# Performance work log

Measured on AMD Instinct MI355X. Metric: run time of the kernel, lower is better.

Reference implementation:

```python
import jax, jax.numpy as jnp
import numpy as np

B, C, Z, E = 2, 32, 4, 2
N = C * C * Z  # 4096 grid points per element
P_TH, T_TH = 0.5, 0.5
ELE_D = (0.74, 0.528)


def _consts():
    real_size = jnp.array([25.0, 25.0, 3.0], jnp.float32)
    lattice = real_size / jnp.array([C, C, Z], jnp.float32)
    g = jnp.stack(jnp.meshgrid(jnp.arange(C), jnp.arange(C), jnp.arange(Z), indexing='ij'), axis=-1)
    pit = g.reshape(N, 3).astype(jnp.float32)
    return pit, lattice


def _cdist(a, b):
    # a [M,3], b [K,3] -> [M,K] euclidean distance
    d2 = jnp.sum((a[:, None, :] - b[None, :, :]) ** 2, axis=-1)
    return jnp.sqrt(d2)


def _nms(pos, conf, valid, ele_d):
    # Fixed-shape version of Analyzer.nms: sort by confidence desc (invalid -> -inf, sorts last),
    # triu(<d) adjacency restricted to valid points, matrix-multiply suppression correction.
    key = jnp.where(valid, conf, -jnp.inf)
    order = jnp.argsort(-key)              # descending confidence
    pos_s = pos[order]
    valid_s = valid[order]
    dist = _cdist(pos_s, pos_s)            # [N,N] ~ 64 MB
    iu = jnp.triu(jnp.ones((N, N), bool), k=1)
    adj = ((dist < ele_d) & iu & valid_s[:, None] & valid_s[None, :]).astype(pos.dtype)
    restrain = adj.sum(0)                  # col sums: # earlier neighbors
    restrain_one = (restrain != 0).astype(pos.dtype)
    correct = restrain_one @ adj           # earlier neighbors that are themselves suppressed
    sel = ((restrain - correct) == 0) & valid_s
    keep = jnp.zeros(N, bool).at[order].set(sel)
    return keep & valid


def _match(t_pos, t_valid, p_pos, p_valid, ele_d):
    # TP matching: T point is matched if any valid P within ele_d; argmin gives its P partner.
    dist = _cdist(t_pos, p_pos)            # [N,N]
    dist = jnp.where(t_valid[:, None] & p_valid[None, :], dist, jnp.inf)
    tp_t_mask = (dist < ele_d).any(1)      # rows in torch's TP_T_index
    tp_p_idx = jnp.argmin(dist, axis=1).astype(jnp.int32)  # torch's TP_P_index (valid where tp_t_mask)
    return tp_t_mask, tp_p_idx


def setup_inputs() -> dict:
    key = jax.random.key(0)
    k1, k2 = jax.random.split(key)
    predictions = jax.random.uniform(k1, (B, C, C, Z, E, 4), jnp.float32)
    targets = jax.random.uniform(k2, (B, C, C, Z, E, 4), jnp.float32)
    return {"predictions": predictions, "targets": targets}


def reference(predictions, targets):
    pit, lattice = _consts()
    # [B,C,C,Z,E,4] -> [B,E,N,4]
    pred = predictions.reshape(B, C, C, Z, E, 4).transpose(0, 4, 1, 2, 3, 5).reshape(B, E, N, 4)
    tgt = targets.reshape(B, C, C, Z, E, 4).transpose(0, 4, 1, 2, 3, 5).reshape(B, E, N, 4)

    p_pos = (pred[..., :3] + pit) * lattice    # [B,E,N,3] absolute coords
    p_conf = pred[..., 3]
    mask_p = p_conf > P_TH
    t_pos = (tgt[..., :3] + pit) * lattice
    mask_t = tgt[..., 3] > T_TH

    keeps, tpt, tpp, tptn, tppn = [], [], [], [], []
    for e in range(E):
        d = ELE_D[e]
        keep_e = jax.vmap(lambda p, c, v: _nms(p, c, v, d))(p_pos[:, e], p_conf[:, e], mask_p[:, e])
        tt, tp = jax.vmap(lambda tq, tv, pq, pv: _match(tq, tv, pq, pv, d))(
            t_pos[:, e], mask_t[:, e], p_pos[:, e], mask_p[:, e])
        ttn, tpn = jax.vmap(lambda tq, tv, pq, pv: _match(tq, tv, pq, pv, d))(
            t_pos[:, e], mask_t[:, e], p_pos[:, e], keep_e)
        keeps.append(keep_e); tpt.append(tt); tpp.append(tp); tptn.append(ttn); tppn.append(tpn)

    keep_nms = jnp.stack(keeps, 1)   # [B,E,N] combined mask_p & nms keep
    tp_t_mask = jnp.stack(tpt, 1)
    tp_p_idx = jnp.stack(tpp, 1)
    tp_t_mask_nms = jnp.stack(tptn, 1)
    tp_p_idx_nms = jnp.stack(tppn, 1)

    return (p_pos, mask_p, keep_nms, t_pos, mask_t,
            tp_t_mask, tp_p_idx, tp_t_mask_nms, tp_p_idx_nms)
```

## Files before the change

kernel.cpp:

```cpp
#include <hip/hip_runtime.h>
#include <cmath>
#include <cstdint>

namespace {
constexpr int NPT  = 4096;
constexpr int NTOT = 16384;

constexpr int O_PPOS  = 0;
constexpr int O_MASKP = 49152;
constexpr int O_KEEP  = 65536;
constexpr int O_TPOS  = 81920;
constexpr int O_MASKT = 131072;
constexpr int O_TPT   = 147456;
constexpr int O_TPP   = 163840;
constexpr int O_TPTN  = 180224;
constexpr int O_TPPN  = 196608;

constexpr size_t W_RESTR = 0;
constexpr size_t W_KEEP  = 16384;
constexpr size_t W_CNT   = 32768;
constexpr size_t W_LIST  = 33024;

constexpr float GUARD = 1.4999f;
}

__device__ __forceinline__ unsigned long long shfl_xor_u64(unsigned long long v, int m) {
    unsigned lo = (unsigned)v, hi = (unsigned)(v >> 32);
    lo = __shfl_xor(lo, m); hi = __shfl_xor(hi, m);
    return ((unsigned long long)hi << 32) | lo;
}
__device__ __forceinline__ unsigned long long shfl_down_u64(unsigned long long v, int m) {
    unsigned lo = (unsigned)v, hi = (unsigned)(v >> 32);
    lo = __shfl_down(lo, m); hi = __shfl_down(hi, m);
    return ((unsigned long long)hi << 32) | lo;
}

__device__ __forceinline__ float3 cellpos(float4 p, int n) {
#pragma clang fp contract(off)
    float fx = (float)(n >> 7), fy = (float)((n >> 2) & 31), fz = (float)(n & 3);
    float3 r;
    r.x = (p.x + fx) * 0.78125f;
    r.y = (p.y + fy) * 0.78125f;
    r.z = (p.z + fz) * 0.75f;
    return r;
}
__device__ __forceinline__ float dist2(float3 a, float3 b) {
#pragma clang fp contract(off)
    float dx = a.x - b.x, dy = a.y - b.y, dz = a.z - b.z;
    float d2 = dx * dx + dy * dy;
    return d2 + dz * dz;
}

__global__ void __launch_bounds__(256) k_restrain(const float4* __restrict__ pred,
                                                  float* __restrict__ out,
                                                  unsigned char* __restrict__ restru,
                                                  unsigned* __restrict__ cnt,
                                                  float s0, float s1) {
#pragma clang fp contract(off)
    int tid = blockIdx.x * 256 + threadIdx.x;
    if (tid == 0) *cnt = 0u;
    int row = tid >> 1, h = tid & 1;
    int n = row & (NPT - 1), s = row >> 12, b = s >> 1, e = s & 1;
    int base4 = b * 8192 + e;
    float se = (s & 1) ? s1 : s0;
    float4 p = pred[base4 + n * 2];
    float3 pj = cellpos(p, n);
    bool valid = p.w > 0.5f;
    if (h == 0) {
        out[O_PPOS + row * 3 + 0] = pj.x;
        out[O_PPOS + row * 3 + 1] = pj.y;
        out[O_PPOS + row * 3 + 2] = pj.z;
        out[O_MASKP + row] = valid ? 1.0f : 0.0f;
    }
    unsigned c = 0;
    if (valid) {
        int gx = n >> 7, gy = (n >> 2) & 31;
        for (int qq = 0; qq < 5; ++qq) {
            int q = qq * 2 + h;
            if (q > 8) continue;
            int nx = gx + q / 3 - 1, ny = gy + q % 3 - 1;
            if ((unsigned)nx > 31u || (unsigned)ny > 31u) continue;
            int nb = nx * 128 + ny * 4;
#pragma unroll
            for (int nz = 0; nz < 4; ++nz) {
                int ni = nb + nz;
                float4 pi = pred[base4 + ni * 2];
                float3 qi = cellpos(pi, ni);
                float d2 = dist2(pj, qi);
                bool prec = (pi.w > p.w) || ((pi.w == p.w) && (ni < n));
                if ((pi.w > 0.5f) && (d2 < se) && prec) c++;
            }
        }
    }
    c += __shfl_xor(c, 1);
    if (h == 0) restru[row] = (unsigned char)c;
}

__global__ void __launch_bounds__(256) k_suppress(const float4* __restrict__ pred,
                                                  const unsigned char* __restrict__ restru,
                                                  float* __restrict__ out,
                                                  unsigned char* __restrict__ keepu,
                                                  float s0, float s1) {
#pragma clang fp contract(off)
    int tid = blockIdx.x * 256 + threadIdx.x;
    int row = tid >> 1, h = tid & 1;
    int n = row & (NPT - 1), s = row >> 12, b = s >> 1, e = s & 1;
    int base4 = b * 8192 + e, srow = s * NPT;
    float se = (s & 1) ? s1 : s0;
    float4 p = pred[base4 + n * 2];
    float3 pj = cellpos(p, n);
    bool valid = p.w > 0.5f;
    unsigned any = 0;
    if (valid) {
        int gx = n >> 7, gy = (n >> 2) & 31;
        for (int qq = 0; qq < 5; ++qq) {
            int q = qq * 2 + h;
            if (q > 8) continue;
            int nx = gx + q / 3 - 1, ny = gy + q % 3 - 1;
            if ((unsigned)nx > 31u || (unsigned)ny > 31u) continue;
            int nb = nx * 128 + ny * 4;
#pragma unroll
            for (int nz = 0; nz < 4; ++nz) {
                int ni = nb + nz;
                float4 pi = pred[base4 + ni * 2];
                float3 qi = cellpos(pi, ni);
                float d2 = dist2(pj, qi);
                bool prec = (pi.w > p.w) || ((pi.w == p.w) && (ni < n));
                bool flg = (pi.w > 0.5f) && (restru[srow + ni] == 0);
                if (flg && (d2 < se) && prec) any = 1u;
            }
        }
    }
    any |= __shfl_xor(any, 1);
    if (h == 0) {
        bool keep = valid && !any;
        out[O_KEEP + row] = keep ? 1.0f : 0.0f;
        keepu[row] = keep ? 1 : 0;
    }
}

__global__ void __launch_bounds__(256) k_match1(const float4* __restrict__ pred,
                                                const float4* __restrict__ tgt,
                                                const unsigned char* __restrict__ keepu,
                                                float* __restrict__ out,
                                                unsigned* __restrict__ list,
                                                unsigned* __restrict__ cnt,
                                                float s0, float s1) {
#pragma clang fp contract(off)
    int tid = blockIdx.x * 256 + threadIdx.x;
    int row = tid >> 2, h = tid & 3;
    int n = row & (NPT - 1), s = row >> 12, b = s >> 1, e = s & 1;
    int base4 = b * 8192 + e, srow = s * NPT;
    float se = (s & 1) ? s1 : s0;
    float4 t4 = tgt[base4 + n * 2];
    float3 tj = cellpos(t4, n);
    bool tv = t4.w > 0.5f;
    if (h == 0) {
        out[O_TPOS + row * 3 + 0] = tj.x;
        out[O_TPOS + row * 3 + 1] = tj.y;
        out[O_TPOS + row * 3 + 2] = tj.z;
        out[O_MASKT + row] = tv ? 1.0f : 0.0f;
    }
    if (!tv) {
        if (h == 0) {
            out[O_TPT + row] = 0.0f; out[O_TPTN + row] = 0.0f;
            out[O_TPP + row] = 0.0f; out[O_TPPN + row] = 0.0f;
        }
        return;
    }
    int gx = n >> 7, gy = (n >> 2) & 31;
    unsigned long long bs = ~0ull, bn = ~0ull;
    unsigned as_ = 0, an_ = 0;
    for (int qq = 0; qq < 7; ++qq) {
        int q = qq * 4 + h;
        if (q > 24) continue;
        int nx = gx + q / 5 - 2, ny = gy + q % 5 - 2;
        if ((unsigned)nx > 31u || (unsigned)ny > 31u) continue;
        int nb = nx * 128 + ny * 4;
#pragma unroll
        for (int nz = 0; nz < 4; ++nz) {
            int ni = nb + nz;
            float4 pi = pred[base4 + ni * 2];
            float3 qi = cellpos(pi, ni);
            float d2 = dist2(tj, qi);
            float dist = sqrtf(d2);
            unsigned long long enc =
                ((unsigned long long)__float_as_uint(dist) << 32) | (unsigned)ni;
            if (pi.w > 0.5f) { if (enc < bs) bs = enc; if (d2 < se) as_ = 1u; }
            if (keepu[srow + ni]) { if (enc < bn) bn = enc; if (d2 < se) an_ = 1u; }
        }
    }
    for (int m = 1; m < 4; m <<= 1) {
        unsigned long long o = shfl_xor_u64(bs, m); if (o < bs) bs = o;
        o = shfl_xor_u64(bn, m); if (o < bn) bn = o;
        as_ |= __shfl_xor(as_, m);
        an_ |= __shfl_xor(an_, m);
    }
    if (h == 0) {
        out[O_TPT + row]  = as_ ? 1.0f : 0.0f;
        out[O_TPTN + row] = an_ ? 1.0f : 0.0f;
        bool acc_s = __uint_as_float((unsigned)(bs >> 32)) < GUARD;
        bool acc_n = __uint_as_float((unsigned)(bn >> 32)) < GUARD;
        if (acc_s) out[O_TPP + row]  = (float)(unsigned)(bs & 0xffffffffull);
        if (acc_n) out[O_TPPN + row] = (float)(unsigned)(bn & 0xffffffffull);
        if (!acc_s || !acc_n) list[atomicAdd(cnt, 1u)] = (unsigned)row;
    }
}

__global__ void __launch_bounds__(256) k_match2(const float4* __restrict__ pred,
                                                const float4* __restrict__ tgt,
                                                const unsigned char* __restrict__ keepu,
                                                const unsigned* __restrict__ list,
                                                const unsigned* __restrict__ cnt,
                                                float* __restrict__ out) {
#pragma clang fp contract(off)
    __shared__ unsigned long long rs[4], rn[4];
    unsigned C = *cnt;
    for (unsigned r = blockIdx.x; r < C; r += gridDim.x) {
        int row = (int)list[r];
        int n = row & (NPT - 1), s = row >> 12, b = s >> 1, e = s & 1;
        int base4 = b * 8192 + e, srow = s * NPT;
        float4 t4 = tgt[base4 + n * 2];
        float3 tj = cellpos(t4, n);
        unsigned long long bs = ~0ull, bn = ~0ull;
        for (int k = (int)threadIdx.x; k < NPT; k += 256) {
            float4 pi = pred[base4 + k * 2];
            float3 qi = cellpos(pi, k);
            float d2 = dist2(tj, qi);
            float dist = sqrtf(d2);
            unsigned long long enc =
                ((unsigned long long)__float_as_uint(dist) << 32) | (unsigned)k;
            if (pi.w > 0.5f && enc < bs) bs = enc;
            if (keepu[srow + k] && enc < bn) bn = enc;
        }
        for (int m = 32; m; m >>= 1) {
            unsigned long long o = shfl_down_u64(bs, m); if (o < bs) bs = o;
            o = shfl_down_u64(bn, m); if (o < bn) bn = o;
        }
        int w = (int)(threadIdx.x >> 6);
        if ((threadIdx.x & 63) == 0) { rs[w] = bs; rn[w] = bn; }
        __syncthreads();
        if (threadIdx.x == 0) {
            for (int i = 1; i < 4; ++i) {
                if (rs[i] < bs) bs = rs[i];
                if (rn[i] < bn) bn = rn[i];
            }
            unsigned is_ = (bs == ~0ull) ? 0u : (unsigned)(bs & 0xffffffffull);
            unsigned in_ = (bn == ~0ull) ? 0u : (unsigned)(bn & 0xffffffffull);
            out[O_TPP + row]  = (float)is_;
            out[O_TPPN + row] = (float)in_;
        }
        __syncthreads();
    }
}

static float sq_boundary(float t) {
    float f = (float)((double)t * (double)t);
    while (sqrtf(f) >= t) f = nextafterf(f, 0.0f);
    while (sqrtf(f) < t)  f = nextafterf(f, __builtin_inff());
    return f;
}

extern "C" void kernel_launch(void* const* d_in, const int* in_sizes, int n_in,
                              void* d_out, int out_size, void* d_ws, size_t ws_size,
                              hipStream_t stream) {
    (void)in_sizes; (void)n_in; (void)out_size; (void)ws_size;
    const float4* pred = (const float4*)d_in[0];
    const float4* tgt  = (const float4*)d_in[1];
    float* out = (float*)d_out;
    char* ws = (char*)d_ws;

    unsigned char* restru = (unsigned char*)(ws + W_RESTR);
    unsigned char* keepu  = (unsigned char*)(ws + W_KEEP);
    unsigned* cnt  = (unsigned*)(ws + W_CNT);
    unsigned* list = (unsigned*)(ws + W_LIST);

    float s0 = sq_boundary(0.74f);
    float s1 = sq_boundary(0.528f);

    k_restrain<<<dim3(128), dim3(256), 0, stream>>>(pred, out, restru, cnt, s0, s1);
    k_suppress<<<dim3(128), dim3(256), 0, stream>>>(pred, restru, out, keepu, s0, s1);
    k_match1 <<<dim3(256), dim3(256), 0, stream>>>(pred, tgt, keepu, out, list, cnt, s0, s1);
    k_match2 <<<dim3(128), dim3(256), 0, stream>>>(pred, tgt, keepu, list, cnt, out);
}
```

Before: 77.90 us.

## Fuse restrain and suppress into one tiled NMS kernel; inline match fallback

Merges the restrain-count and suppression kernels into one kernel per tile. Each block recomputes restrain counts for its tile plus a one-cell halo in shared memory, so the global restrain buffer and one launch go away. The two match kernels are also merged: rows whose local-neighbourhood best match is not guaranteed now do the full-grid scan in the same 4-lane group instead of being queued with an atomic and handled by a second kernel. This cuts four launches to two, at the cost of redundant halo work and a possibly long serial scan for the rare fallback rows.

```diff
diff --git a/kernel.cpp b/kernel.cpp
--- a/kernel.cpp
+++ b/kernel.cpp
@@ -4,7 +4,6 @@
 
 namespace {
 constexpr int NPT  = 4096;
-constexpr int NTOT = 16384;
 
 constexpr int O_PPOS  = 0;
 constexpr int O_MASKP = 49152;
@@ -16,22 +15,12 @@
 constexpr int O_TPTN  = 180224;
 constexpr int O_TPPN  = 196608;
 
-constexpr size_t W_RESTR = 0;
-constexpr size_t W_KEEP  = 16384;
-constexpr size_t W_CNT   = 32768;
-constexpr size_t W_LIST  = 33024;
-
 constexpr float GUARD = 1.4999f;
 }
 
 __device__ __forceinline__ unsigned long long shfl_xor_u64(unsigned long long v, int m) {
     unsigned lo = (unsigned)v, hi = (unsigned)(v >> 32);
     lo = __shfl_xor(lo, m); hi = __shfl_xor(hi, m);
-    return ((unsigned long long)hi << 32) | lo;
-}
-__device__ __forceinline__ unsigned long long shfl_down_u64(unsigned long long v, int m) {
-    unsigned lo = (unsigned)v, hi = (unsigned)(v >> 32);
-    lo = __shfl_down(lo, m); hi = __shfl_down(hi, m);
     return ((unsigned long long)hi << 32) | lo;
 }
 
@@ -51,36 +40,66 @@
     return d2 + dz * dz;
 }
 
-__global__ void __launch_bounds__(256) k_restrain(const float4* __restrict__ pred,
-                                                  float* __restrict__ out,
-                                                  unsigned char* __restrict__ restru,
-                                                  unsigned* __restrict__ cnt,
-                                                  float s0, float s1) {
-#pragma clang fp contract(off)
-    int tid = blockIdx.x * 256 + threadIdx.x;
-    if (tid == 0) *cnt = 0u;
-    int row = tid >> 1, h = tid & 1;
-    int n = row & (NPT - 1), s = row >> 12, b = s >> 1, e = s & 1;
+__global__ void __launch_bounds__(256) k_nms(const float4* __restrict__ pred,
+                                             float* __restrict__ out,
+                                             unsigned char* __restrict__ keepu,
+                                             float s0, float s1) {
+#pragma clang fp contract(off)
+    __shared__ unsigned char restr[216];
+    int bid = blockIdx.x;
+    int h2 = bid & 1, gx = (bid >> 1) & 31, s = bid >> 6;
+    int b = s >> 1, e = s & 1;
     int base4 = b * 8192 + e;
     float se = (s & 1) ? s1 : s0;
+    int gy0 = h2 << 4;
+    int t = (int)threadIdx.x;
+
+    if (t < 216) {
+        int rgx = t / 72, rem = t - rgx * 72, rgy = rem >> 2, z = rem & 3;
+        int px = gx + rgx - 1, py = gy0 + rgy - 1;
+        unsigned c = 0;
+        if ((unsigned)px < 32u && (unsigned)py < 32u) {
+            int pn = px * 128 + py * 4 + z;
+            float4 p = pred[base4 + pn * 2];
+            if (p.w > 0.5f) {
+                float3 pj = cellpos(p, pn);
+                for (int q = 0; q < 9; ++q) {
+                    int nx = px + q / 3 - 1, ny = py + q % 3 - 1;
+                    if ((unsigned)nx > 31u || (unsigned)ny > 31u) continue;
+                    int nb = nx * 128 + ny * 4;
+#pragma unroll
+                    for (int nz = 0; nz < 4; ++nz) {
+                        int ni = nb + nz;
+                        float4 pi = pred[base4 + ni * 2];
+                        float3 qi = cellpos(pi, ni);
+                        float d2 = dist2(pj, qi);
+                        bool prec = (pi.w > p.w) || ((pi.w == p.w) && (ni < pn));
+                        if ((pi.w > 0.5f) && (d2 < se) && prec) c++;
+                    }
+                }
+            }
+        }
+        restr[t] = (unsigned char)c;
+    }
+    __syncthreads();
+
+    int r = t >> 2, h = t & 3;
+    int gy = gy0 + (r >> 2), z = r & 3;
+    int n = (gx << 7) + (gy << 2) + z;
+    int row = s * NPT + n;
     float4 p = pred[base4 + n * 2];
     float3 pj = cellpos(p, n);
     bool valid = p.w > 0.5f;
-    if (h == 0) {
-        out[O_PPOS + row * 3 + 0] = pj.x;
-        out[O_PPOS + row * 3 + 1] = pj.y;
-        out[O_PPOS + row * 3 + 2] = pj.z;
-        out[O_MASKP + row] = valid ? 1.0f : 0.0f;
-    }
-    unsigned c = 0;
+    unsigned any = 0;
     if (valid) {
-        int gx = n >> 7, gy = (n >> 2) & 31;
-        for (int qq = 0; qq < 5; ++qq) {
-            int q = qq * 2 + h;
+        for (int qq = 0; qq < 3; ++qq) {
+            int q = qq * 4 + h;
             if (q > 8) continue;
-            int nx = gx + q / 3 - 1, ny = gy + q % 3 - 1;
+            int dx = q / 3 - 1, dy = q % 3 - 1;
+            int nx = gx + dx, ny = gy + dy;
             if ((unsigned)nx > 31u || (unsigned)ny > 31u) continue;
             int nb = nx * 128 + ny * 4;
+            const unsigned char* lr = &restr[(dx + 1) * 72 + (gy - gy0 + dy + 1) * 4];
 #pragma unroll
             for (int nz = 0; nz < 4; ++nz) {
                 int ni = nb + nz;
@@ -88,66 +107,31 @@
                 float3 qi = cellpos(pi, ni);
                 float d2 = dist2(pj, qi);
                 bool prec = (pi.w > p.w) || ((pi.w == p.w) && (ni < n));
-                if ((pi.w > 0.5f) && (d2 < se) && prec) c++;
-            }
-        }
-    }
-    c += __shfl_xor(c, 1);
-    if (h == 0) restru[row] = (unsigned char)c;
-}
-
-__global__ void __launch_bounds__(256) k_suppress(const float4* __restrict__ pred,
-                                                  const unsigned char* __restrict__ restru,
-                                                  float* __restrict__ out,
-                                                  unsigned char* __restrict__ keepu,
-                                                  float s0, float s1) {
-#pragma clang fp contract(off)
-    int tid = blockIdx.x * 256 + threadIdx.x;
-    int row = tid >> 1, h = tid & 1;
-    int n = row & (NPT - 1), s = row >> 12, b = s >> 1, e = s & 1;
-    int base4 = b * 8192 + e, srow = s * NPT;
-    float se = (s & 1) ? s1 : s0;
-    float4 p = pred[base4 + n * 2];
-    float3 pj = cellpos(p, n);
-    bool valid = p.w > 0.5f;
-    unsigned any = 0;
-    if (valid) {
-        int gx = n >> 7, gy = (n >> 2) & 31;
-        for (int qq = 0; qq < 5; ++qq) {
-            int q = qq * 2 + h;
-            if (q > 8) continue;
-            int nx = gx + q / 3 - 1, ny = gy + q % 3 - 1;
-            if ((unsigned)nx > 31u || (unsigned)ny > 31u) continue;
-            int nb = nx * 128 + ny * 4;
-#pragma unroll
-            for (int nz = 0; nz < 4; ++nz) {
-                int ni = nb + nz;
-                float4 pi = pred[base4 + ni * 2];
-                float3 qi = cellpos(pi, ni);
-                float d2 = dist2(pj, qi);
-                bool prec = (pi.w > p.w) || ((pi.w == p.w) && (ni < n));
-                bool flg = (pi.w > 0.5f) && (restru[srow + ni] == 0);
+                bool flg = (pi.w > 0.5f) && (lr[nz] == 0);
                 if (flg && (d2 < se) && prec) any = 1u;
             }
         }
     }
     any |= __shfl_xor(any, 1);
+    any |= __shfl_xor(any, 2);
     if (h == 0) {
+        out[O_PPOS + row * 3 + 0] = pj.x;
+        out[O_PPOS + row * 3 + 1] = pj.y;
+        out[O_PPOS + row * 3 + 2] = pj.z;
+        out[O_MASKP + row] = valid ? 1.0f : 0.0f;
         bool keep = valid && !any;
         out[O_KEEP + row] = keep ? 1.0f : 0.0f;
         keepu[row] = keep ? 1 : 0;
     }
 }
 
-__global__ void __launch_bounds__(256) k_match1(const float4* __restrict__ pred,
-                                                const float4* __restrict__ tgt,
-                                                const unsigned char* __restrict__ keepu,
-                                                float* __restrict__ out,
-                                                unsigned* __restrict__ list,
-                                                unsigned* __restrict__ cnt,
-                                                float s0, float s1) {
-#pragma clang fp contract(off)
-    int tid = blockIdx.x * 256 + threadIdx.x;
+__global__ void __launch_bounds__(256) k_match(const float4* __restrict__ pred,
+                                               const float4* __restrict__ tgt,
+                                               const unsigned char* __restrict__ keepu,
+                                               float* __restrict__ out,
+                                               float s0, float s1) {
+#pragma clang fp contract(off)
+    int tid = blockIdx.x * 256 + (int)threadIdx.x;
     int row = tid >> 2, h = tid & 3;
     int n = row & (NPT - 1), s = row >> 12, b = s >> 1, e = s & 1;
     int base4 = b * 8192 + e, srow = s * NPT;
@@ -196,61 +180,31 @@
         as_ |= __shfl_xor(as_, m);
         an_ |= __shfl_xor(an_, m);
     }
-    if (h == 0) {
-        out[O_TPT + row]  = as_ ? 1.0f : 0.0f;
-        out[O_TPTN + row] = an_ ? 1.0f : 0.0f;
-        bool acc_s = __uint_as_float((unsigned)(bs >> 32)) < GUARD;
-        bool acc_n = __uint_as_float((unsigned)(bn >> 32)) < GUARD;
-        if (acc_s) out[O_TPP + row]  = (float)(unsigned)(bs & 0xffffffffull);
-        if (acc_n) out[O_TPPN + row] = (float)(unsigned)(bn & 0xffffffffull);
-        if (!acc_s || !acc_n) list[atomicAdd(cnt, 1u)] = (unsigned)row;
-    }
-}
-
-__global__ void __launch_bounds__(256) k_match2(const float4* __restrict__ pred,
-                                                const float4* __restrict__ tgt,
-                                                const unsigned char* __restrict__ keepu,
-                                                const unsigned* __restrict__ list,
-                                                const unsigned* __restrict__ cnt,
-                                                float* __restrict__ out) {
-#pragma clang fp contract(off)
-    __shared__ unsigned long long rs[4], rn[4];
-    unsigned C = *cnt;
-    for (unsigned r = blockIdx.x; r < C; r += gridDim.x) {
-        int row = (int)list[r];
-        int n = row & (NPT - 1), s = row >> 12, b = s >> 1, e = s & 1;
-        int base4 = b * 8192 + e, srow = s * NPT;
-        float4 t4 = tgt[base4 + n * 2];
-        float3 tj = cellpos(t4, n);
-        unsigned long long bs = ~0ull, bn = ~0ull;
-        for (int k = (int)threadIdx.x; k < NPT; k += 256) {
+    bool acc_s = __uint_as_float((unsigned)(bs >> 32)) < GUARD;
+    bool acc_n = __uint_as_float((unsigned)(bn >> 32)) < GUARD;
+    if (!(acc_s && acc_n)) {
+        unsigned long long fs = ~0ull, fn = ~0ull;
+        for (int k = h; k < NPT; k += 4) {
             float4 pi = pred[base4 + k * 2];
             float3 qi = cellpos(pi, k);
             float d2 = dist2(tj, qi);
             float dist = sqrtf(d2);
             unsigned long long enc =
                 ((unsigned long long)__float_as_uint(dist) << 32) | (unsigned)k;
-            if (pi.w > 0.5f && enc < bs) bs = enc;
-            if (keepu[srow + k] && enc < bn) bn = enc;
-        }
-        for (int m = 32; m; m >>= 1) {
-            unsigned long long o = shfl_down_u64(bs, m); if (o < bs) bs = o;
-            o = shfl_down_u64(bn, m); if (o < bn) bn = o;
-        }
-        int w = (int)(threadIdx.x >> 6);
-        if ((threadIdx.x & 63) == 0) { rs[w] = bs; rn[w] = bn; }
-        __syncthreads();
-        if (threadIdx.x == 0) {
-            for (int i = 1; i < 4; ++i) {
-                if (rs[i] < bs) bs = rs[i];
-                if (rn[i] < bn) bn = rn[i];
-            }
-            unsigned is_ = (bs == ~0ull) ? 0u : (unsigned)(bs & 0xffffffffull);
-            unsigned in_ = (bn == ~0ull) ? 0u : (unsigned)(bn & 0xffffffffull);
-            out[O_TPP + row]  = (float)is_;
-            out[O_TPPN + row] = (float)in_;
-        }
-        __syncthreads();
+            if (pi.w > 0.5f && enc < fs) fs = enc;
+            if (keepu[srow + k] && enc < fn) fn = enc;
+        }
+        for (int m = 1; m < 4; m <<= 1) {
+            unsigned long long o = shfl_xor_u64(fs, m); if (o < fs) fs = o;
+            o = shfl_xor_u64(fn, m); if (o < fn) fn = o;
+        }
+        bs = fs; bn = fn;
+    }
+    if (h == 0) {
+        out[O_TPT + row]  = as_ ? 1.0f : 0.0f;
+        out[O_TPTN + row] = an_ ? 1.0f : 0.0f;
+        out[O_TPP + row]  = (float)((bs == ~0ull) ? 0u : (unsigned)(bs & 0xffffffffull));
+        out[O_TPPN + row] = (float)((bn == ~0ull) ? 0u : (unsigned)(bn & 0xffffffffull));
     }
 }
 
@@ -268,18 +222,11 @@
     const float4* pred = (const float4*)d_in[0];
     const float4* tgt  = (const float4*)d_in[1];
     float* out = (float*)d_out;
-    char* ws = (char*)d_ws;
-
-    unsigned char* restru = (unsigned char*)(ws + W_RESTR);
-    unsigned char* keepu  = (unsigned char*)(ws + W_KEEP);
-    unsigned* cnt  = (unsigned*)(ws + W_CNT);
-    unsigned* list = (unsigned*)(ws + W_LIST);
+    unsigned char* keepu = (unsigned char*)d_ws;
 
     float s0 = sq_boundary(0.74f);
     float s1 = sq_boundary(0.528f);
 
-    k_restrain<<<dim3(128), dim3(256), 0, stream>>>(pred, out, restru, cnt, s0, s1);
-    k_suppress<<<dim3(128), dim3(256), 0, stream>>>(pred, restru, out, keepu, s0, s1);
-    k_match1 <<<dim3(256), dim3(256), 0, stream>>>(pred, tgt, keepu, out, list, cnt, s0, s1);
-    k_match2 <<<dim3(128), dim3(256), 0, stream>>>(pred, tgt, keepu, list, cnt, out);
-}
+    k_nms  <<<dim3(256), dim3(256), 0, stream>>>(pred, out, keepu, s0, s1);
+    k_match<<<dim3(256), dim3(256), 0, stream>>>(pred, tgt, keepu, out, s0, s1);
+}
```

Measured after the change: 75.77 us. 1.03x faster.
